# Kernel tuning notes

Hardware: AMD Instinct MI355X
Metric: run time of the kernel (lower is better)

Reference implementation:

```python
import jax, jax.numpy as jnp
import numpy as np


def setup_inputs() -> dict:
    key = jax.random.key(0)
    ks = jax.random.split(key, 16)
    B, D, H = 65536, 64, 512
    s = 0.05
    inp = {
        "state": jax.random.normal(ks[0], (B, D), dtype=jnp.float32),
        "Wz0": jax.random.normal(ks[1], (H, D), dtype=jnp.float32) * s,
        "bz0": jax.random.normal(ks[2], (H,), dtype=jnp.float32) * s,
        "Wz1": jax.random.normal(ks[3], (H, H), dtype=jnp.float32) * s,
        "Wz2": jax.random.normal(ks[4], (H, H), dtype=jnp.float32) * s,
        "Wz3": jax.random.normal(ks[5], (H, H), dtype=jnp.float32) * s,
        "WzL": jax.random.normal(ks[6], (1, H), dtype=jnp.float32) * s,
        "Wx0": jax.random.normal(ks[7], (H, D), dtype=jnp.float32) * s,
        "bx0": jax.random.normal(ks[8], (H,), dtype=jnp.float32) * s,
        "Wx1": jax.random.normal(ks[9], (H, D), dtype=jnp.float32) * s,
        "bx1": jax.random.normal(ks[10], (H,), dtype=jnp.float32) * s,
        "Wx2": jax.random.normal(ks[11], (H, D), dtype=jnp.float32) * s,
        "bx2": jax.random.normal(ks[12], (H,), dtype=jnp.float32) * s,
        "WxL": jax.random.normal(ks[13], (1, D), dtype=jnp.float32) * s,
    }
    return inp


def reference(state, Wz0, bz0, Wz1, Wz2, Wz3, WzL, Wx0, bx0, Wx1, bx1, Wx2, bx2, WxL):
    sp = jax.nn.softplus

    def icnn_sum(x):  # x: [B, D] -> scalar (sum of per-sample convex outputs)
        z = sp(x @ Wz0.T + bz0)                      # [B, H]
        z = sp(z @ Wz1.T + x @ Wx0.T + bx0)          # [B, H]
        z = sp(z @ Wz2.T + x @ Wx1.T + bx1)          # [B, H]
        z = sp(z @ Wz3.T + x @ Wx2.T + bx2)          # [B, H]
        out = z @ WzL.T + x @ WxL.T                  # [B, 1]
        return out.sum()

    x = state - 1.0
    # Output is scalar per-sample, so grad of the batch-sum equals the stacked
    # per-sample jacobians computed by the torch Python loop.
    action = jax.grad(icnn_sum)(x)                   # [B, D]
    return action
```

## Files before the change

### kernel.cpp

```cpp
#include <hip/hip_runtime.h>

typedef unsigned short u16;
typedef unsigned int u32;
typedef unsigned long long u64;

#define B_TOTAL 65536
#define H 512
#define D 64
#define BM 64
#define CH 520

typedef __bf16 bf16x8 __attribute__((ext_vector_type(8)));
typedef float f32x4 __attribute__((ext_vector_type(4)));
typedef float f32x16 __attribute__((ext_vector_type(16)));

__device__ __forceinline__ u32 f2b(float f) {
  u32 u = __builtin_bit_cast(u32, f);
  return (u + 0x7fffu + ((u >> 16) & 1u)) >> 16;
}
__device__ __forceinline__ u16 f2bc(float f) {
  return __builtin_bit_cast(u16, (__bf16)f);
}
__device__ __forceinline__ float b2f(u32 bits) {
  return __builtin_bit_cast(float, bits << 16);
}

#define OFF_Wz0b 0
#define OFF_Wx0b 32768
#define OFF_Wx1b 65536
#define OFF_Wx2b 98304
#define OFF_Wz1b 131072
#define OFF_Wz2b 393216
#define OFF_Wz3b 655360
#define OFF_Wz1t 917504
#define OFF_Wz2t 1179648
#define OFF_Wz3t 1441792
#define OFF_Wz0t 1703936
#define OFF_Wx0t 1736704
#define OFF_Wx1t 1769472
#define OFF_Wx2t 1802240
#define OFF_WEND 1835008
#define WS_ELEMS OFF_WEND

__global__ __launch_bounds__(256) void prep_kernel(
    const float* __restrict__ Wz0, const float* __restrict__ Wz1,
    const float* __restrict__ Wz2, const float* __restrict__ Wz3,
    const float* __restrict__ Wx0, const float* __restrict__ Wx1,
    const float* __restrict__ Wx2, u16* __restrict__ wsb) {
  int i = blockIdx.x * 256 + threadIdx.x;
  const float* src;
  int NN, KK, trans, p;
  if (i < 131072) {
    int r = i >> 15; p = i & 32767;
    src = (r == 0) ? Wz0 : (r == 1) ? Wx0 : (r == 2) ? Wx1 : Wx2;
    NN = 512; KK = 64; trans = 0;
  } else if (i < 917504) {
    int j = i - 131072; int r = j >> 18; p = j & 262143;
    src = (r == 0) ? Wz1 : (r == 1) ? Wz2 : Wz3;
    NN = 512; KK = 512; trans = 0;
  } else if (i < 1703936) {
    int j = i - 917504; int r = j >> 18; p = j & 262143;
    src = (r == 0) ? Wz1 : (r == 1) ? Wz2 : Wz3;
    NN = 512; KK = 512; trans = 1;
  } else {
    int j = i - 1703936; int r = j >> 15; p = j & 32767;
    src = (r == 0) ? Wz0 : (r == 1) ? Wx0 : (r == 2) ? Wx1 : Wx2;
    NN = 64; KK = 512; trans = 1;
  }
  int jj = p & 7, lane = (p >> 3) & 63, blk = p >> 9;
  int kt_sh = (KK == 64) ? 2 : 5;
  int ntile = blk >> kt_sh;
  int kstep = blk & ((1 << kt_sh) - 1);
  int n = ntile * 32 + (lane & 31);
  int k = kstep * 16 + ((lane >> 5) << 3) + jj;
  float v = trans ? src[k * NN + n] : src[n * KK + k];
  wsb[i] = (u16)f2b(v);
}

__global__ __launch_bounds__(256) void fill_sentinel(float* out, int n) {
  int i = blockIdx.x * 256 + threadIdx.x;
  if (i < n) out[i] = 12345.0f;
}

__global__ __launch_bounds__(1024, 4) void icnn_kernel(
    const float* __restrict__ state,
    const float* __restrict__ bz0, const float* __restrict__ bx0,
    const float* __restrict__ bx1, const float* __restrict__ bx2,
    const float* __restrict__ WzL, const float* __restrict__ WxL,
    u16* __restrict__ wsw, float* __restrict__ out) {
  __shared__ u16 zbA[64 * CH];
  __shared__ u16 zbB[64 * CH];
  __shared__ u16 xbuf[BM * 72];

  const int tid = threadIdx.x;
  const int w = tid >> 6;
  const int lane = tid & 63;
  const int l31 = lane & 31;
  const int q5 = lane >> 5;
  const int blk = blockIdx.x;

  const u16* Wz0b = wsw + OFF_Wz0b;
  const u16* Wx0b = wsw + OFF_Wx0b;
  const u16* Wx1b = wsw + OFF_Wx1b;
  const u16* Wx2b = wsw + OFF_Wx2b;
  const u16* Wz1b = wsw + OFF_Wz1b;
  const u16* Wz2b = wsw + OFF_Wz2b;
  const u16* Wz3b = wsw + OFF_Wz3b;
  const u16* Wz1t = wsw + OFF_Wz1t;
  const u16* Wz2t = wsw + OFF_Wz2t;
  const u16* Wz3t = wsw + OFF_Wz3t;
  const u16* Wz0t = wsw + OFF_Wz0t;
  const u16* Wx0t = wsw + OFF_Wx0t;
  const u16* Wx1t = wsw + OFF_Wx1t;
  const u16* Wx2t = wsw + OFF_Wx2t;

  auto lbar = [&]() {
    asm volatile("s_waitcnt lgkmcnt(0)" ::: "memory");
    __builtin_amdgcn_s_barrier();
    asm volatile("" ::: "memory");
  };

  {
    int r = tid >> 4, c0 = (tid & 15) << 2;
    const float* p = state + (blk * BM + r) * D + c0;
    f32x4 v = __builtin_nontemporal_load((const f32x4*)p);
    u32* dst = (u32*)&xbuf[r * 72 + c0];
    dst[0] = (u32)f2bc(v[0] - 1.0f) | ((u32)f2bc(v[1] - 1.0f) << 16);
    dst[1] = (u32)f2bc(v[2] - 1.0f) | ((u32)f2bc(v[3] - 1.0f) << 16);
  }

  const f32x16 Z16 = {0,0,0,0,0,0,0,0,0,0,0,0,0,0,0,0};
  f32x16 acc[2];
  f32x16 pk = Z16;
  u64 sg0[8], sg1[8], sg2[8];

  auto ldA = [&](const u16* zb, int rt, int ks) -> bf16x8 {
    return *(const bf16x8*)(&zb[(ks * 2 + rt) * CH + lane * 8]);
  };
  auto ldX = [&](int rt, int ks) -> bf16x8 {
    return *(const bf16x8*)(&xbuf[(rt * 32 + l31) * 72 + ks * 16 + q5 * 8]);
  };

  auto fwdX = [&](const u16* Wxp) {
    const u16* xb = Wxp + (w * 4) * 512 + lane * 8;
#pragma unroll
    for (int ks = 0; ks < 4; ++ks) {
      bf16x8 b = *(const bf16x8*)(xb + ks * 512);
      bf16x8 a0 = ldX(0, ks);
      bf16x8 a1 = ldX(1, ks);
      acc[0] = __builtin_amdgcn_mfma_f32_32x32x16_bf16(a0, b, (ks == 0) ? Z16 : acc[0], 0, 0, 0);
      acc[1] = __builtin_amdgcn_mfma_f32_32x32x16_bf16(a1, b, (ks == 0) ? Z16 : acc[1], 0, 0, 0);
    }
  };

  auto fwdH = [&](const u16* Wp, const u16* zb) {
    const u16* gb = Wp + (w * 32) * 512 + lane * 8;
    bf16x8 b0 = *(const bf16x8*)(gb);
    bf16x8 b1 = *(const bf16x8*)(gb + 512);
#pragma unroll 2
    for (int st = 0; st < 32; ++st) {
      int stp = (st < 30) ? st + 2 : st;
      bf16x8 bn = *(const bf16x8*)(gb + stp * 512);
      bf16x8 a0 = ldA(zb, 0, st);
      bf16x8 a1 = ldA(zb, 1, st);
      __builtin_amdgcn_s_setprio(1);
      acc[0] = __builtin_amdgcn_mfma_f32_32x32x16_bf16(a0, b0, acc[0], 0, 0, 0);
      acc[1] = __builtin_amdgcn_mfma_f32_32x32x16_bf16(a1, b0, acc[1], 0, 0, 0);
      __builtin_amdgcn_s_setprio(0);
      b0 = b1; b1 = bn;
    }
  };
  auto zeroAcc = [&]() { acc[0] = Z16; acc[1] = Z16; };

  const int C0 = (2 * w + (l31 >> 4)) * (2 * CH) + ((l31 >> 3) & 1) * 256 + (l31 & 7);

  auto fwd_epi = [&](const float* biasp, u64 (&sg)[8], u16* zb) {
    float bias = biasp[w * 32 + l31];
#pragma unroll
    for (int rt = 0; rt < 2; ++rt)
#pragma unroll
      for (int g = 0; g < 4; ++g) {
        u64 pack = 0;
#pragma unroll
        for (int e = 0; e < 4; ++e) {
          float a = acc[rt][g * 4 + e] + bias;
          float t = __expf(-a);
          float u = 1.0f + t;
          float s = __builtin_amdgcn_rcpf(u);
          float z = a + __logf(u);
          pack |= (u64)f2bc(s) << (16 * e);
          zb[C0 + rt * CH + (e + 8 * g + 4 * q5) * 8] = f2bc(z);
        }
        sg[rt * 4 + g] = pack;
      }
  };
  auto d3_epi = [&](const float* biasp, u16* zb) {
    float bias = biasp[w * 32 + l31];
    float wl = WzL[w * 32 + l31];
#pragma unroll
    for (int rt = 0; rt < 2; ++rt)
#pragma unroll
      for (int g = 0; g < 4; ++g)
#pragma unroll
        for (int e = 0; e < 4; ++e) {
          float a = acc[rt][g * 4 + e] + bias;
          float t = __expf(-a);
          float s = __builtin_amdgcn_rcpf(1.0f + t);
          zb[C0 + rt * CH + (e + 8 * g + 4 * q5) * 8] = f2bc(wl * s);
        }
  };
  auto bwd_epi = [&](const u64 (&sg)[8], u16* zb) {
#pragma unroll
    for (int rt = 0; rt < 2; ++rt)
#pragma unroll
      for (int g = 0; g < 4; ++g) {
        u64 v = sg[rt * 4 + g];
#pragma unroll
        for (int e = 0; e < 4; ++e) {
          float s = b2f((u32)(v >> (16 * e)) & 0xffffu);
          float d = acc[rt][g * 4 + e] * s;
          zb[C0 + rt * CH + (e + 8 * g + 4 * q5) * 8] = f2bc(d);
        }
      }
  };

  auto minigrad = [&](const u16* Wg, const u16* zb, bool init) {
    int tr = w & 1, tc = (w >> 1) & 1, kq = w >> 2;
    const u16* gb = Wg + (tc * 32 + kq * 8) * 512 + lane * 8;
    f32x16 t = pk;
    if (init) t = Z16;
#pragma unroll 2
    for (int i = 0; i < 8; ++i) {
      bf16x8 a = ldA(zb, tr, kq * 8 + i);
      bf16x8 g = *(const bf16x8*)(gb + i * 512);
      __builtin_amdgcn_s_setprio(1);
      t = __builtin_amdgcn_mfma_f32_32x32x16_bf16(a, g, t, 0, 0, 0);
      __builtin_amdgcn_s_setprio(0);
    }
    pk = t;
  };

  lbar();
  fwdX(Wz0b);
  fwd_epi(bz0, sg0, zbA);
  lbar();
  fwdX(Wx0b); fwdH(Wz1b, zbA);
  fwd_epi(bx0, sg1, zbB);
  lbar();
  fwdX(Wx1b); fwdH(Wz2b, zbB);
  fwd_epi(bx1, sg2, zbA);
  lbar();
  fwdX(Wx2b); fwdH(Wz3b, zbA);
  d3_epi(bx2, zbB);
  lbar();
  minigrad(Wx2t, zbB, true);
  zeroAcc(); fwdH(Wz3t, zbB);
  bwd_epi(sg2, zbA);
  lbar();
  minigrad(Wx1t, zbA, false);
  zeroAcc(); fwdH(Wz2t, zbA);
  bwd_epi(sg1, zbB);
  lbar();
  minigrad(Wx0t, zbB, false);
  zeroAcc(); fwdH(Wz1t, zbB);
  bwd_epi(sg0, zbA);
  lbar();
  minigrad(Wz0t, zbA, false);
  {
    float* park = (float*)zbB;
#pragma unroll
    for (int reg = 0; reg < 16; ++reg)
      park[(w * 16 + reg) * 64 + lane] = pk[reg];
  }
  lbar();
  {
    int t = w & 3, rg = w >> 2;
    int tr = t & 1, tc = (t >> 1) & 1;
    int col = tc * 32 + l31;
    float wx = WxL[col];
    const float* park = (const float*)zbB;
#pragma unroll
    for (int e = 0; e < 4; ++e) {
      int reg = rg * 4 + e;
      float v = park[(t * 16 + reg) * 64 + lane]
              + park[((t + 4) * 16 + reg) * 64 + lane]
              + park[((t + 8) * 16 + reg) * 64 + lane]
              + park[((t + 12) * 16 + reg) * 64 + lane];
      int row = blk * BM + tr * 32 + e + 8 * rg + 4 * q5;
      out[row * D + col] = v + wx;
    }
  }
}

extern "C" void kernel_launch(void* const* d_in, const int* in_sizes, int n_in,
                              void* d_out, int out_size, void* d_ws, size_t ws_size,
                              hipStream_t stream) {
  const float* state = (const float*)d_in[0];
  const float* Wz0 = (const float*)d_in[1];
  const float* bz0 = (const float*)d_in[2];
  const float* Wz1 = (const float*)d_in[3];
  const float* Wz2 = (const float*)d_in[4];
  const float* Wz3 = (const float*)d_in[5];
  const float* WzL = (const float*)d_in[6];
  const float* Wx0 = (const float*)d_in[7];
  const float* bx0 = (const float*)d_in[8];
  const float* Wx1 = (const float*)d_in[9];
  const float* bx1 = (const float*)d_in[10];
  const float* Wx2 = (const float*)d_in[11];
  const float* bx2 = (const float*)d_in[12];
  const float* WxL = (const float*)d_in[13];

  if (ws_size < (size_t)WS_ELEMS * 2) {
    fill_sentinel<<<(out_size + 255) / 256, 256, 0, stream>>>((float*)d_out, out_size);
    return;
  }
  u16* wsw = (u16*)d_ws;
  prep_kernel<<<OFF_WEND / 256, 256, 0, stream>>>(Wz0, Wz1, Wz2, Wz3, Wx0, Wx1, Wx2, wsw);
  icnn_kernel<<<B_TOTAL / BM, 1024, 0, stream>>>(state, bz0, bx0, bx1, bx2, WzL, WxL,
                                                 wsw, (float*)d_out);
}
```

Before: 414.0 us.

## Double batch tile to 128 rows with single LDS buffer and global sigmoid slabs

Raises the batch tile from 64 to 128 rows so each wave runs four MFMA row tiles per weight fragment, halving weight reloads per sample. To fit in LDS it replaces the two ping-pong activation buffers with one in-place buffer, which needs extra barriers between the GEMM and epilogue phases. Sigmoid derivatives that were kept in registers are now written to global workspace slabs and read back in the backward pass, which frees registers but adds global memory traffic. The grid is halved, so there are fewer blocks to spread across the GPU.

```diff
diff --git a/kernel.cpp b/kernel.cpp
--- a/kernel.cpp
+++ b/kernel.cpp
@@ -7,7 +7,7 @@
 #define B_TOTAL 65536
 #define H 512
 #define D 64
-#define BM 64
+#define BM 128
 #define CH 520
 
 typedef __bf16 bf16x8 __attribute__((ext_vector_type(8)));
@@ -40,7 +40,11 @@
 #define OFF_Wx1t 1769472
 #define OFF_Wx2t 1802240
 #define OFF_WEND 1835008
-#define WS_ELEMS OFF_WEND
+#define SLAB_ELEMS (B_TOTAL * H)
+#define OFF_S0 OFF_WEND
+#define OFF_S1 (OFF_S0 + SLAB_ELEMS)
+#define OFF_S2 (OFF_S1 + SLAB_ELEMS)
+#define WS_ELEMS (OFF_S2 + SLAB_ELEMS)
 
 __global__ __launch_bounds__(256) void prep_kernel(
     const float* __restrict__ Wz0, const float* __restrict__ Wz1,
@@ -88,8 +92,7 @@
     const float* __restrict__ bx1, const float* __restrict__ bx2,
     const float* __restrict__ WzL, const float* __restrict__ WxL,
     u16* __restrict__ wsw, float* __restrict__ out) {
-  __shared__ u16 zbA[64 * CH];
-  __shared__ u16 zbB[64 * CH];
+  __shared__ u16 zbuf[128 * CH];
   __shared__ u16 xbuf[BM * 72];
 
   const int tid = threadIdx.x;
@@ -113,6 +116,9 @@
   const u16* Wx0t = wsw + OFF_Wx0t;
   const u16* Wx1t = wsw + OFF_Wx1t;
   const u16* Wx2t = wsw + OFF_Wx2t;
+  u64* slab0 = (u64*)(wsw + OFF_S0);
+  u64* slab1 = (u64*)(wsw + OFF_S1);
+  u64* slab2 = (u64*)(wsw + OFF_S2);
 
   auto lbar = [&]() {
     asm volatile("s_waitcnt lgkmcnt(0)" ::: "memory");
@@ -121,21 +127,24 @@
   };
 
   {
-    int r = tid >> 4, c0 = (tid & 15) << 2;
-    const float* p = state + (blk * BM + r) * D + c0;
-    f32x4 v = __builtin_nontemporal_load((const f32x4*)p);
-    u32* dst = (u32*)&xbuf[r * 72 + c0];
-    dst[0] = (u32)f2bc(v[0] - 1.0f) | ((u32)f2bc(v[1] - 1.0f) << 16);
-    dst[1] = (u32)f2bc(v[2] - 1.0f) | ((u32)f2bc(v[3] - 1.0f) << 16);
+#pragma unroll
+    for (int ii = 0; ii < 2; ++ii) {
+      int i = tid * 2 + ii;
+      int r = i >> 4, c0 = (i & 15) << 2;
+      const float* p = state + (blk * BM + r) * D + c0;
+      f32x4 v = __builtin_nontemporal_load((const f32x4*)p);
+      u32* dst = (u32*)&xbuf[r * 72 + c0];
+      dst[0] = (u32)f2bc(v[0] - 1.0f) | ((u32)f2bc(v[1] - 1.0f) << 16);
+      dst[1] = (u32)f2bc(v[2] - 1.0f) | ((u32)f2bc(v[3] - 1.0f) << 16);
+    }
   }
 
   const f32x16 Z16 = {0,0,0,0,0,0,0,0,0,0,0,0,0,0,0,0};
-  f32x16 acc[2];
+  f32x16 acc[4];
   f32x16 pk = Z16;
-  u64 sg0[8], sg1[8], sg2[8];
-
-  auto ldA = [&](const u16* zb, int rt, int ks) -> bf16x8 {
-    return *(const bf16x8*)(&zb[(ks * 2 + rt) * CH + lane * 8]);
+
+  auto ldA = [&](int rt, int ks) -> bf16x8 {
+    return *(const bf16x8*)(&zbuf[(ks * 4 + rt) * CH + lane * 8]);
   };
   auto ldX = [&](int rt, int ks) -> bf16x8 {
     return *(const bf16x8*)(&xbuf[(rt * 32 + l31) * 72 + ks * 16 + q5 * 8]);
@@ -146,14 +155,16 @@
 #pragma unroll
     for (int ks = 0; ks < 4; ++ks) {
       bf16x8 b = *(const bf16x8*)(xb + ks * 512);
-      bf16x8 a0 = ldX(0, ks);
-      bf16x8 a1 = ldX(1, ks);
-      acc[0] = __builtin_amdgcn_mfma_f32_32x32x16_bf16(a0, b, (ks == 0) ? Z16 : acc[0], 0, 0, 0);
-      acc[1] = __builtin_amdgcn_mfma_f32_32x32x16_bf16(a1, b, (ks == 0) ? Z16 : acc[1], 0, 0, 0);
+#pragma unroll
+      for (int rt = 0; rt < 4; ++rt) {
+        bf16x8 a = ldX(rt, ks);
+        acc[rt] = __builtin_amdgcn_mfma_f32_32x32x16_bf16(
+            a, b, (ks == 0) ? Z16 : acc[rt], 0, 0, 0);
+      }
     }
   };
 
-  auto fwdH = [&](const u16* Wp, const u16* zb) {
+  auto fwdH = [&](const u16* Wp) {
     const u16* gb = Wp + (w * 32) * 512 + lane * 8;
     bf16x8 b0 = *(const bf16x8*)(gb);
     bf16x8 b1 = *(const bf16x8*)(gb + 512);
@@ -161,23 +172,31 @@
     for (int st = 0; st < 32; ++st) {
       int stp = (st < 30) ? st + 2 : st;
       bf16x8 bn = *(const bf16x8*)(gb + stp * 512);
-      bf16x8 a0 = ldA(zb, 0, st);
-      bf16x8 a1 = ldA(zb, 1, st);
+      bf16x8 a0 = ldA(0, st);
+      bf16x8 a1 = ldA(1, st);
+      bf16x8 a2 = ldA(2, st);
+      bf16x8 a3 = ldA(3, st);
       __builtin_amdgcn_s_setprio(1);
       acc[0] = __builtin_amdgcn_mfma_f32_32x32x16_bf16(a0, b0, acc[0], 0, 0, 0);
       acc[1] = __builtin_amdgcn_mfma_f32_32x32x16_bf16(a1, b0, acc[1], 0, 0, 0);
+      acc[2] = __builtin_amdgcn_mfma_f32_32x32x16_bf16(a2, b0, acc[2], 0, 0, 0);
+      acc[3] = __builtin_amdgcn_mfma_f32_32x32x16_bf16(a3, b0, acc[3], 0, 0, 0);
       __builtin_amdgcn_s_setprio(0);
       b0 = b1; b1 = bn;
     }
   };
-  auto zeroAcc = [&]() { acc[0] = Z16; acc[1] = Z16; };
-
-  const int C0 = (2 * w + (l31 >> 4)) * (2 * CH) + ((l31 >> 3) & 1) * 256 + (l31 & 7);
-
-  auto fwd_epi = [&](const float* biasp, u64 (&sg)[8], u16* zb) {
+  auto zeroAcc = [&]() {
+#pragma unroll
+    for (int rt = 0; rt < 4; ++rt) acc[rt] = Z16;
+  };
+
+  const int C0 = (w * 2 + (l31 >> 4)) * 4 * CH + ((l31 >> 3) & 1) * 256 +
+                 q5 * 32 + (l31 & 7);
+
+  auto fwd_epi = [&](const float* biasp, u64* slab) {
     float bias = biasp[w * 32 + l31];
 #pragma unroll
-    for (int rt = 0; rt < 2; ++rt)
+    for (int rt = 0; rt < 4; ++rt)
 #pragma unroll
       for (int g = 0; g < 4; ++g) {
         u64 pack = 0;
@@ -189,16 +208,16 @@
           float s = __builtin_amdgcn_rcpf(u);
           float z = a + __logf(u);
           pack |= (u64)f2bc(s) << (16 * e);
-          zb[C0 + rt * CH + (e + 8 * g + 4 * q5) * 8] = f2bc(z);
+          zbuf[C0 + rt * CH + (e + 8 * g) * 8] = f2bc(z);
         }
-        sg[rt * 4 + g] = pack;
+        slab[((blk * 16 + w) * 16 + rt * 4 + g) * 64 + lane] = pack;
       }
   };
-  auto d3_epi = [&](const float* biasp, u16* zb) {
+  auto d3_epi = [&](const float* biasp) {
     float bias = biasp[w * 32 + l31];
     float wl = WzL[w * 32 + l31];
 #pragma unroll
-    for (int rt = 0; rt < 2; ++rt)
+    for (int rt = 0; rt < 4; ++rt)
 #pragma unroll
       for (int g = 0; g < 4; ++g)
 #pragma unroll
@@ -206,89 +225,95 @@
           float a = acc[rt][g * 4 + e] + bias;
           float t = __expf(-a);
           float s = __builtin_amdgcn_rcpf(1.0f + t);
-          zb[C0 + rt * CH + (e + 8 * g + 4 * q5) * 8] = f2bc(wl * s);
+          zbuf[C0 + rt * CH + (e + 8 * g) * 8] = f2bc(wl * s);
         }
   };
-  auto bwd_epi = [&](const u64 (&sg)[8], u16* zb) {
-#pragma unroll
-    for (int rt = 0; rt < 2; ++rt)
+  auto bwd_epi = [&](const u64* slab) {
+#pragma unroll
+    for (int rt = 0; rt < 4; ++rt)
 #pragma unroll
       for (int g = 0; g < 4; ++g) {
-        u64 v = sg[rt * 4 + g];
+        u64 v = slab[((blk * 16 + w) * 16 + rt * 4 + g) * 64 + lane];
 #pragma unroll
         for (int e = 0; e < 4; ++e) {
           float s = b2f((u32)(v >> (16 * e)) & 0xffffu);
           float d = acc[rt][g * 4 + e] * s;
-          zb[C0 + rt * CH + (e + 8 * g + 4 * q5) * 8] = f2bc(d);
+          zbuf[C0 + rt * CH + (e + 8 * g) * 8] = f2bc(d);
         }
       }
   };
 
-  auto minigrad = [&](const u16* Wg, const u16* zb, bool init) {
-    int tr = w & 1, tc = (w >> 1) & 1, kq = w >> 2;
-    const u16* gb = Wg + (tc * 32 + kq * 8) * 512 + lane * 8;
-    f32x16 t = pk;
-    if (init) t = Z16;
+  auto minigrad = [&](const u16* Wg, bool init) {
+    int t = w & 7, kh = w >> 3;
+    int tr = t & 3, tc = t >> 2;
+    const u16* gb = Wg + (tc * 32 + kh * 16) * 512 + lane * 8;
+    f32x16 acu = pk;
+    if (init) acu = Z16;
 #pragma unroll 2
-    for (int i = 0; i < 8; ++i) {
-      bf16x8 a = ldA(zb, tr, kq * 8 + i);
+    for (int i = 0; i < 16; ++i) {
+      bf16x8 a = ldA(tr, kh * 16 + i);
       bf16x8 g = *(const bf16x8*)(gb + i * 512);
       __builtin_amdgcn_s_setprio(1);
-      t = __builtin_amdgcn_mfma_f32_32x32x16_bf16(a, g, t, 0, 0, 0);
+      acu = __builtin_amdgcn_mfma_f32_32x32x16_bf16(a, g, acu, 0, 0, 0);
       __builtin_amdgcn_s_setprio(0);
     }
-    pk = t;
+    pk = acu;
   };
 
   lbar();
   fwdX(Wz0b);
-  fwd_epi(bz0, sg0, zbA);
-  lbar();
-  fwdX(Wx0b); fwdH(Wz1b, zbA);
-  fwd_epi(bx0, sg1, zbB);
-  lbar();
-  fwdX(Wx1b); fwdH(Wz2b, zbB);
-  fwd_epi(bx1, sg2, zbA);
-  lbar();
-  fwdX(Wx2b); fwdH(Wz3b, zbA);
-  d3_epi(bx2, zbB);
-  lbar();
-  minigrad(Wx2t, zbB, true);
-  zeroAcc(); fwdH(Wz3t, zbB);
-  bwd_epi(sg2, zbA);
-  lbar();
-  minigrad(Wx1t, zbA, false);
-  zeroAcc(); fwdH(Wz2t, zbA);
-  bwd_epi(sg1, zbB);
-  lbar();
-  minigrad(Wx0t, zbB, false);
-  zeroAcc(); fwdH(Wz1t, zbB);
-  bwd_epi(sg0, zbA);
-  lbar();
-  minigrad(Wz0t, zbA, false);
-  {
-    float* park = (float*)zbB;
+  fwd_epi(bz0, slab0);
+  lbar();
+  fwdX(Wx0b); fwdH(Wz1b);
+  lbar();
+  fwd_epi(bx0, slab1);
+  lbar();
+  fwdX(Wx1b); fwdH(Wz2b);
+  lbar();
+  fwd_epi(bx1, slab2);
+  lbar();
+  fwdX(Wx2b); fwdH(Wz3b);
+  lbar();
+  d3_epi(bx2);
+  lbar();
+  minigrad(Wx2t, true);
+  zeroAcc(); fwdH(Wz3t);
+  lbar();
+  bwd_epi(slab2);
+  lbar();
+  minigrad(Wx1t, false);
+  zeroAcc(); fwdH(Wz2t);
+  lbar();
+  bwd_epi(slab1);
+  lbar();
+  minigrad(Wx0t, false);
+  zeroAcc(); fwdH(Wz1t);
+  lbar();
+  bwd_epi(slab0);
+  lbar();
+  minigrad(Wz0t, false);
+  lbar();
+  if (w >= 8) {
+    float* park = (float*)zbuf;
 #pragma unroll
     for (int reg = 0; reg < 16; ++reg)
-      park[(w * 16 + reg) * 64 + lane] = pk[reg];
-  }
-  lbar();
-  {
-    int t = w & 3, rg = w >> 2;
-    int tr = t & 1, tc = (t >> 1) & 1;
+      park[((w - 8) * 16 + reg) * 64 + lane] = pk[reg];
+  }
+  lbar();
+  if (w < 8) {
+    int tr = w & 3, tc = w >> 2;
     int col = tc * 32 + l31;
     float wx = WxL[col];
-    const float* park = (const float*)zbB;
-#pragma unroll
-    for (int e = 0; e < 4; ++e) {
-      int reg = rg * 4 + e;
-      float v = park[(t * 16 + reg) * 64 + lane]
-              + park[((t + 4) * 16 + reg) * 64 + lane]
-              + park[((t + 8) * 16 + reg) * 64 + lane]
-              + park[((t + 12) * 16 + reg) * 64 + lane];
-      int row = blk * BM + tr * 32 + e + 8 * rg + 4 * q5;
-      out[row * D + col] = v + wx;
-    }
+    const float* park = (const float*)zbuf;
+#pragma unroll
+    for (int g = 0; g < 4; ++g)
+#pragma unroll
+      for (int e = 0; e < 4; ++e) {
+        int reg = g * 4 + e;
+        float v = pk[reg] + park[(w * 16 + reg) * 64 + lane];
+        int row = blk * BM + tr * 32 + e + 8 * g + 4 * q5;
+        out[row * D + col] = v + wx;
+      }
   }
 }
 
```

New measurement: 446.8 us. +7.9%, slower.
